# Performance work log

Measured on AMD Instinct MI355X. Metric: run time of the kernel, lower is better.

The kernel has to match this reference:

```python
import jax, jax.numpy as jnp
import numpy as np

DT = 0.1  # discretization step (matches init kwarg dt)


def setup_inputs() -> dict:
    key = jax.random.key(0)
    k1, k2, k3, k4 = jax.random.split(key, 4)
    Bsz, L, D, N = 16, 4096, 128, 64
    x = jax.random.normal(k1, (Bsz, L, D), dtype=jnp.float32)
    # torch uses torch.rand for A; shift by -N*I so A is Hurwitz and the
    # 4096-step recurrence stays numerically stable (same math, stable init).
    A = jax.random.uniform(k2, (D, N, N), dtype=jnp.float32) - float(N) * jnp.eye(N, dtype=jnp.float32)
    B = jax.random.uniform(k3, (D, N, 1), dtype=jnp.float32)
    C = jax.random.uniform(k4, (D, 1, N), dtype=jnp.float32)
    return {"x": x, "A": A, "B": B, "C": C}


def _discretize(A, B):
    # Bilinear (Tustin) transform, per channel d: [D, N, N]
    N = A.shape[-1]
    I = jnp.eye(N, dtype=A.dtype)[None, :, :]
    inv = jnp.linalg.inv(I - A * (DT / 2))
    A_bar = inv @ (I + A * (DT / 2))          # [D, N, N]
    B_bar = (inv @ B) * DT                    # [D, N, 1]
    return A_bar, B_bar


def reference(x, A, B, C):
    # x: [Bsz, L, D]; A: [D, N, N]; B: [D, N, 1]; C: [D, 1, N]
    Bsz, L, D = x.shape
    N = A.shape[-1]
    A_bar, B_bar = _discretize(A, B)
    Bb = B_bar[:, :, 0]                       # [D, N]
    Cv = C[:, 0, :]                           # [D, N]
    xs = jnp.moveaxis(x, 1, 0)                # [L, Bsz, D]
    h0 = jnp.zeros((Bsz, D, N), dtype=x.dtype)

    def step(h, x_t):
        # h_new[b,d,m] = sum_n A_bar[d,m,n] h[b,d,n] + x_t[b,d] * Bb[d,m]
        h = jnp.einsum('dmn,bdn->bdm', A_bar, h) + x_t[:, :, None] * Bb[None]
        y_t = jnp.einsum('bdn,dn->bd', h, Cv)
        return h, y_t

    _, ys = jax.lax.scan(step, h0, xs)        # ys: [L, Bsz, D]
    return jnp.moveaxis(ys, 0, 1)             # [Bsz, L, D]
```

## Files before the change

kernel.cpp:

```cpp
#include <hip/hip_runtime.h>

typedef float f4 __attribute__((ext_vector_type(4)));

#define PAD 68
#define ALPHA 0.29f

__device__ __forceinline__ void mm_acc(const float* L, const float* R,
                                       int i0, int j0, float acc[16]) {
  #pragma unroll
  for (int m = 0; m < 16; ++m) acc[m] = 0.f;
  #pragma unroll
  for (int n = 0; n < 64; n += 4) {
    f4 La[4], Rb[4];
    #pragma unroll
    for (int m = 0; m < 4; ++m) La[m] = *(const f4*)&L[(i0 + m) * PAD + n];
    #pragma unroll
    for (int p = 0; p < 4; ++p) Rb[p] = *(const f4*)&R[(n + p) * PAD + j0];
    #pragma unroll
    for (int m = 0; m < 4; ++m)
      #pragma unroll
      for (int p = 0; p < 4; ++p)
        #pragma unroll
        for (int c = 0; c < 4; ++c)
          acc[m * 4 + c] += La[m][p] * Rb[p][c];
  }
}

__global__ __launch_bounds__(256) void s4_discretize(
    const float* __restrict__ Ag,
    const float* __restrict__ Bg,
    const float* __restrict__ Cg,
    float* __restrict__ Kout)
{
  __shared__ float Ms[64 * PAD];
  __shared__ float Xs[64 * PAD];
  __shared__ float Ts[64 * PAD];
  __shared__ float C4[4][65];
  __shared__ float U16[64][16];
  __shared__ float Bv[64], Cv0[64], Bb[64];
  __shared__ float Pr[4][64];

  const int d   = blockIdx.x;
  const int tid = threadIdx.x;
  const int i0  = (tid >> 4) << 2;
  const int j0  = (tid & 15) << 2;
  const int q   = tid >> 6;
  const int ln  = tid & 63;

  for (int idx = tid; idx < 4096; idx += 256) {
    int i = idx >> 6, j = idx & 63;
    float a = Ag[(size_t)d * 4096 + idx];
    float m = ((i == j) ? 1.f : 0.f) - 0.05f * a;
    Ms[i * PAD + j] = m;
    Xs[i * PAD + j] = ((i == j) ? 2.f * ALPHA : 0.f) - ALPHA * ALPHA * m;
  }
  if (tid < 64) { Bv[tid] = Bg[d * 64 + tid]; Cv0[tid] = Cg[d * 64 + tid]; }
  __syncthreads();

  float acc[16];
  for (int it = 0; it < 2; ++it) {
    mm_acc(Ms, Xs, i0, j0, acc);
    #pragma unroll
    for (int m = 0; m < 4; ++m) {
      f4 t = {acc[m*4+0], acc[m*4+1], acc[m*4+2], acc[m*4+3]};
      *(f4*)&Ts[(i0 + m) * PAD + j0] = t;
    }
    __syncthreads();
    mm_acc(Xs, Ts, i0, j0, acc);
    __syncthreads();
    #pragma unroll
    for (int m = 0; m < 4; ++m) {
      f4 xo = *(const f4*)&Xs[(i0 + m) * PAD + j0];
      f4 t = {acc[m*4+0], acc[m*4+1], acc[m*4+2], acc[m*4+3]};
      *(f4*)&Xs[(i0 + m) * PAD + j0] = 2.f * xo - t;
    }
    __syncthreads();
  }

  {
    float p = 0.f;
    #pragma unroll
    for (int m = 0; m < 16; ++m) p += Xs[ln * PAD + q * 16 + m] * Bv[q * 16 + m];
    Pr[q][ln] = p;
  }
  for (int idx = tid; idx < 4096; idx += 256) {
    int i = idx >> 6, j = idx & 63;
    Ms[i * PAD + j] = 2.f * Xs[i * PAD + j] - ((i == j) ? 1.f : 0.f);
  }
  __syncthreads();
  if (tid < 64) Bb[tid] = 0.1f * (Pr[0][tid] + Pr[1][tid] + Pr[2][tid] + Pr[3][tid]);
  __syncthreads();

  if (tid < 64) C4[0][tid] = Cv0[tid];
  __syncthreads();
  for (int j = 1; j < 4; ++j) {
    float p = 0.f;
    #pragma unroll
    for (int m = 0; m < 16; ++m) p += C4[j - 1][q * 16 + m] * Ms[(q * 16 + m) * PAD + ln];
    Pr[q][ln] = p;
    __syncthreads();
    if (q == 0) C4[j][ln] = Pr[0][ln] + Pr[1][ln] + Pr[2][ln] + Pr[3][ln];
    __syncthreads();
  }

  mm_acc(Ms, Ms, i0, j0, acc);
  #pragma unroll
  for (int m = 0; m < 4; ++m) {
    f4 t = {acc[m*4+0], acc[m*4+1], acc[m*4+2], acc[m*4+3]};
    *(f4*)&Ts[(i0 + m) * PAD + j0] = t;
  }
  __syncthreads();
  mm_acc(Ts, Ts, i0, j0, acc);
  __syncthreads();
  #pragma unroll
  for (int m = 0; m < 4; ++m) {
    f4 t = {acc[m*4+0], acc[m*4+1], acc[m*4+2], acc[m*4+3]};
    *(f4*)&Xs[(i0 + m) * PAD + j0] = t;
  }
  __syncthreads();

  if (tid < 64) U16[tid][0] = Bb[tid];
  __syncthreads();
  for (int i = 1; i < 16; ++i) {
    float p = 0.f;
    #pragma unroll
    for (int m = 0; m < 16; ++m) p += Xs[ln * PAD + q * 16 + m] * U16[q * 16 + m][i - 1];
    Pr[q][ln] = p;
    __syncthreads();
    if (q == 0) U16[ln][i] = Pr[0][ln] + Pr[1][ln] + Pr[2][ln] + Pr[3][ln];
    __syncthreads();
  }

  if (tid < 64) {
    int i = tid >> 2, j = tid & 3;
    float s = 0.f;
    #pragma unroll
    for (int n = 0; n < 64; ++n) s += C4[j][n] * U16[n][i];
    Kout[tid * 128 + d] = s;
  }
}

__global__ __launch_bounds__(256) void s4_conv(
    const float* __restrict__ xg,
    const float* __restrict__ Ktg,
    float* __restrict__ yg)
{
  __shared__ float xs[319 * 32];
  __shared__ float Ks[64 * 32];

  const int tid = threadIdx.y * 32 + threadIdx.x;
  const int tc  = blockIdx.x;
  const int dq  = blockIdx.y;
  const int b   = blockIdx.z;
  const int d0  = dq * 32;
  const int t0  = tc * 256;

  for (int idx = tid; idx < 2048; idx += 256)
    Ks[idx] = Ktg[(idx >> 5) * 128 + d0 + (idx & 31)];

  const float* xb = xg + (size_t)b * 4096 * 128 + d0;
  for (int idx = tid; idx < 319 * 8; idx += 256) {
    int row = idx >> 3, c4 = (idx & 7) << 2;
    int t = t0 - 63 + row;
    f4 v = {0.f, 0.f, 0.f, 0.f};
    if (t >= 0) v = *(const f4*)&xb[(size_t)t * 128 + c4];
    *(f4*)&xs[row * 32 + c4] = v;
  }
  __syncthreads();

  const int dl = threadIdx.x;
  const int g  = threadIdx.y;

  float acc[32];
  #pragma unroll
  for (int t = 0; t < 32; ++t) acc[t] = 0.f;

  float w[47];
  #pragma unroll
  for (int k0 = 0; k0 < 64; k0 += 16) {
    const int base = g * 32 + 48 - k0;
    #pragma unroll
    for (int jj = 0; jj < 47; ++jj) w[jj] = xs[(base + jj) * 32 + dl];
    #pragma unroll
    for (int k = k0; k < k0 + 16; ++k) {
      float kv = Ks[k * 32 + dl];
      #pragma unroll
      for (int t = 0; t < 32; ++t)
        acc[t] += kv * w[t + (k0 + 15 - k)];
    }
  }

  float* yb = yg + ((size_t)b * 4096 + t0 + g * 32) * 128 + d0 + dl;
  #pragma unroll
  for (int t = 0; t < 32; ++t)
    yb[(size_t)t * 128] = acc[t];
}

extern "C" void kernel_launch(void* const* d_in, const int* in_sizes, int n_in,
                              void* d_out, int out_size, void* d_ws, size_t ws_size,
                              hipStream_t stream) {
  const float* x = (const float*)d_in[0];
  const float* A = (const float*)d_in[1];
  const float* B = (const float*)d_in[2];
  const float* C = (const float*)d_in[3];
  float* y  = (float*)d_out;
  float* Kt = (float*)d_ws;

  s4_discretize<<<128, 256, 0, stream>>>(A, B, C, Kt);
  dim3 grid(16, 4, 16), block(32, 8);
  s4_conv<<<grid, block, 0, stream>>>(x, Kt, y);
}
```

Measured before the change: 124.6 us.

## Use polynomial seed for Newton inverse and restructure Krylov power computations

Replaces the scalar Newton-Schulz seed with a quadratic polynomial in M, which needs one extra matrix square but allows dropping one Newton iteration. It also computes the M^8 power ahead of time so that the 16-step B-vector Krylov chain becomes 4 serial steps plus 3 batched steps, and it computes the C-vector powers in two stages. Together these cut the number of serialized syncthreads-bound matvec stages in the discretize kernel. The cost is an extra 64x68 shared buffer and some risk to accuracy if the polynomial seed converges less well than two Newton iterations.

```diff
diff --git a/kernel.cpp b/kernel.cpp
--- a/kernel.cpp
+++ b/kernel.cpp
@@ -3,7 +3,10 @@
 typedef float f4 __attribute__((ext_vector_type(4)));
 
 #define PAD 68
-#define ALPHA 0.29f
+
+#define SEED_C2 0.0251681f
+#define SEED_C1 (-0.262380f)
+#define SEED_C0 0.895613f
 
 __device__ __forceinline__ void mm_acc(const float* L, const float* R,
                                        int i0, int j0, float acc[16]) {
@@ -23,6 +26,14 @@
         #pragma unroll
         for (int c = 0; c < 4; ++c)
           acc[m * 4 + c] += La[m][p] * Rb[p][c];
+  }
+}
+
+__device__ __forceinline__ void store_tile(float* Dst, int i0, int j0, const float acc[16]) {
+  #pragma unroll
+  for (int m = 0; m < 4; ++m) {
+    f4 t = {acc[m*4+0], acc[m*4+1], acc[m*4+2], acc[m*4+3]};
+    *(f4*)&Dst[(i0 + m) * PAD + j0] = t;
   }
 }
 
@@ -35,8 +46,9 @@
   __shared__ float Ms[64 * PAD];
   __shared__ float Xs[64 * PAD];
   __shared__ float Ts[64 * PAD];
-  __shared__ float C4[4][65];
-  __shared__ float U16[64][16];
+  __shared__ float Qs[64 * PAD];
+  __shared__ float C4[4][PAD];
+  __shared__ float U16[16][PAD];
   __shared__ float Bv[64], Cv0[64], Bb[64];
   __shared__ float Pr[4][64];
 
@@ -47,35 +59,49 @@
   const int q   = tid >> 6;
   const int ln  = tid & 63;
 
+  {
+    const f4* Af = (const f4*)(Ag + (size_t)d * 4096);
+    #pragma unroll
+    for (int s = 0; s < 4; ++s) {
+      int idx4 = tid + s * 256;
+      int i = idx4 >> 4, jb = (idx4 & 15) << 2;
+      f4 a = Af[idx4];
+      f4 m;
+      #pragma unroll
+      for (int c = 0; c < 4; ++c)
+        m[c] = ((i == jb + c) ? 1.f : 0.f) - 0.05f * a[c];
+      *(f4*)&Ms[i * PAD + jb] = m;
+    }
+  }
+  if (tid < 64) { Bv[tid] = Bg[d * 64 + tid]; Cv0[tid] = Cg[d * 64 + tid]; }
+  __syncthreads();
+
+  float acc[16];
+
+  mm_acc(Ms, Ms, i0, j0, acc);
+  store_tile(Ts, i0, j0, acc);
+  __syncthreads();
+
   for (int idx = tid; idx < 4096; idx += 256) {
     int i = idx >> 6, j = idx & 63;
-    float a = Ag[(size_t)d * 4096 + idx];
-    float m = ((i == j) ? 1.f : 0.f) - 0.05f * a;
-    Ms[i * PAD + j] = m;
-    Xs[i * PAD + j] = ((i == j) ? 2.f * ALPHA : 0.f) - ALPHA * ALPHA * m;
-  }
-  if (tid < 64) { Bv[tid] = Bg[d * 64 + tid]; Cv0[tid] = Cg[d * 64 + tid]; }
-  __syncthreads();
-
-  float acc[16];
-  for (int it = 0; it < 2; ++it) {
-    mm_acc(Ms, Xs, i0, j0, acc);
-    #pragma unroll
-    for (int m = 0; m < 4; ++m) {
-      f4 t = {acc[m*4+0], acc[m*4+1], acc[m*4+2], acc[m*4+3]};
-      *(f4*)&Ts[(i0 + m) * PAD + j0] = t;
-    }
-    __syncthreads();
-    mm_acc(Xs, Ts, i0, j0, acc);
-    __syncthreads();
-    #pragma unroll
-    for (int m = 0; m < 4; ++m) {
-      f4 xo = *(const f4*)&Xs[(i0 + m) * PAD + j0];
-      f4 t = {acc[m*4+0], acc[m*4+1], acc[m*4+2], acc[m*4+3]};
-      *(f4*)&Xs[(i0 + m) * PAD + j0] = 2.f * xo - t;
-    }
-    __syncthreads();
-  }
+    float v = SEED_C2 * Ts[i * PAD + j] + SEED_C1 * Ms[i * PAD + j]
+            + ((i == j) ? SEED_C0 : 0.f);
+    Xs[i * PAD + j] = v;
+  }
+  __syncthreads();
+
+  mm_acc(Ms, Xs, i0, j0, acc);
+  store_tile(Ts, i0, j0, acc);
+  __syncthreads();
+  mm_acc(Xs, Ts, i0, j0, acc);
+  __syncthreads();
+  #pragma unroll
+  for (int m = 0; m < 4; ++m) {
+    f4 xo = *(const f4*)&Xs[(i0 + m) * PAD + j0];
+    f4 t = {acc[m*4+0], acc[m*4+1], acc[m*4+2], acc[m*4+3]};
+    *(f4*)&Xs[(i0 + m) * PAD + j0] = 2.f * xo - t;
+  }
+  __syncthreads();
 
   {
     float p = 0.f;
@@ -87,56 +113,74 @@
     int i = idx >> 6, j = idx & 63;
     Ms[i * PAD + j] = 2.f * Xs[i * PAD + j] - ((i == j) ? 1.f : 0.f);
   }
-  __syncthreads();
+  if (tid < 64) C4[0][tid] = Cv0[tid];
+  __syncthreads();
+
   if (tid < 64) Bb[tid] = 0.1f * (Pr[0][tid] + Pr[1][tid] + Pr[2][tid] + Pr[3][tid]);
-  __syncthreads();
-
-  if (tid < 64) C4[0][tid] = Cv0[tid];
-  __syncthreads();
-  for (int j = 1; j < 4; ++j) {
-    float p = 0.f;
-    #pragma unroll
-    for (int m = 0; m < 16; ++m) p += C4[j - 1][q * 16 + m] * Ms[(q * 16 + m) * PAD + ln];
-    Pr[q][ln] = p;
+  mm_acc(Ms, Ms, i0, j0, acc);
+  store_tile(Ts, i0, j0, acc);
+  __syncthreads();
+
+  mm_acc(Ts, Ts, i0, j0, acc);
+  __syncthreads();
+  store_tile(Xs, i0, j0, acc);
+  if (tid < 64) U16[0][tid] = Bb[tid];
+  __syncthreads();
+
+  mm_acc(Xs, Xs, i0, j0, acc);
+  store_tile(Qs, i0, j0, acc);
+
+  __syncthreads();
+  if (tid < 64) {
+    float s = 0.f;
+    #pragma unroll
+    for (int m = 0; m < 64; ++m) s += C4[0][m] * Ms[m * PAD + tid];
+    C4[1][tid] = s;
+  }
+  __syncthreads();
+
+  if (tid < 128) {
+    int j = 2 + (tid >> 6), n = tid & 63;
+    float s = 0.f;
+    #pragma unroll
+    for (int m = 0; m < 64; ++m) s += C4[j - 2][m] * Ts[m * PAD + n];
+    C4[j][n] = s;
+  }
+  __syncthreads();
+
+  for (int i = 1; i < 4; ++i) {
+    if (tid < 64) {
+      f4 s = {0.f, 0.f, 0.f, 0.f};
+      const f4* Arow = (const f4*)&Xs[tid * PAD];
+      const f4* uv   = (const f4*)&U16[i - 1][0];
+      #pragma unroll
+      for (int m = 0; m < 16; ++m) s += Arow[m] * uv[m];
+      U16[i][tid] = s[0] + s[1] + s[2] + s[3];
+    }
     __syncthreads();
-    if (q == 0) C4[j][ln] = Pr[0][ln] + Pr[1][ln] + Pr[2][ln] + Pr[3][ln];
+  }
+
+  #pragma unroll
+  for (int base = 0; base < 12; base += 4) {
+    int v = tid >> 6, n = tid & 63;
+    f4 s = {0.f, 0.f, 0.f, 0.f};
+    const f4* Arow = (const f4*)&Qs[n * PAD];
+    const f4* uv   = (const f4*)&U16[base + v][0];
+    #pragma unroll
+    for (int m = 0; m < 16; ++m) s += Arow[m] * uv[m];
     __syncthreads();
-  }
-
-  mm_acc(Ms, Ms, i0, j0, acc);
-  #pragma unroll
-  for (int m = 0; m < 4; ++m) {
-    f4 t = {acc[m*4+0], acc[m*4+1], acc[m*4+2], acc[m*4+3]};
-    *(f4*)&Ts[(i0 + m) * PAD + j0] = t;
-  }
-  __syncthreads();
-  mm_acc(Ts, Ts, i0, j0, acc);
-  __syncthreads();
-  #pragma unroll
-  for (int m = 0; m < 4; ++m) {
-    f4 t = {acc[m*4+0], acc[m*4+1], acc[m*4+2], acc[m*4+3]};
-    *(f4*)&Xs[(i0 + m) * PAD + j0] = t;
-  }
-  __syncthreads();
-
-  if (tid < 64) U16[tid][0] = Bb[tid];
-  __syncthreads();
-  for (int i = 1; i < 16; ++i) {
-    float p = 0.f;
-    #pragma unroll
-    for (int m = 0; m < 16; ++m) p += Xs[ln * PAD + q * 16 + m] * U16[q * 16 + m][i - 1];
-    Pr[q][ln] = p;
-    __syncthreads();
-    if (q == 0) U16[ln][i] = Pr[0][ln] + Pr[1][ln] + Pr[2][ln] + Pr[3][ln];
+    U16[base + 4 + v][n] = s[0] + s[1] + s[2] + s[3];
     __syncthreads();
   }
 
   if (tid < 64) {
     int i = tid >> 2, j = tid & 3;
-    float s = 0.f;
-    #pragma unroll
-    for (int n = 0; n < 64; ++n) s += C4[j][n] * U16[n][i];
-    Kout[tid * 128 + d] = s;
+    f4 s = {0.f, 0.f, 0.f, 0.f};
+    const f4* cj = (const f4*)&C4[j][0];
+    const f4* ui = (const f4*)&U16[i][0];
+    #pragma unroll
+    for (int n = 0; n < 16; ++n) s += cj[n] * ui[n];
+    Kout[tid * 128 + d] = s[0] + s[1] + s[2] + s[3];
   }
 }
 
```

Result: slower. 131.8 us (+5.8%).
